# Kernel tuning notes

Measured on AMD Instinct MI355X. Metric: run time of the kernel, lower is better.

The kernel has to match this reference:

```python
import jax, jax.numpy as jnp
import numpy as np

N, T, D, H, E, ED = 4096, 16, 5, 128, 32768, 32

def _leaky(x):
    return jnp.where(x >= 0, x, 0.2 * x)

def _lstm(x, Wih, Whh, bih, bhh):
    # x: [N, T, D] -> hidden sequence [N, T, H]; PyTorch gate order i,f,g,o
    pre = jnp.einsum('ntd,gd->tng', x, Wih) + bih + bhh  # [T, N, 4H]
    Hd = Whh.shape[1]
    def step(carry, p):
        h, c = carry
        g = p + h @ Whh.T
        i, f, gg, o = jnp.split(g, 4, axis=-1)
        c = jax.nn.sigmoid(f) * c + jax.nn.sigmoid(i) * jnp.tanh(gg)
        h = jax.nn.sigmoid(o) * jnp.tanh(c)
        return (h, c), h
    z = jnp.zeros((x.shape[0], Hd), x.dtype)
    _, hs = jax.lax.scan(step, (z, z), pre)
    return jnp.swapaxes(hs, 0, 1)

def _sire(x, src, dst, efeat, Wq, bq, Wk, bk, We, be, Wr, br):
    # SIREConv with agg_type='sum': m = LeakyReLU(eq[dst]+ek[src]+e); sum over in-edges; then linear_relation
    eq = x @ Wq.T + bq            # [N, T, H]
    ek = x @ Wk.T + bk            # [N, T, H]
    e = efeat @ We.T + be         # [E, H]
    m = _leaky(eq[dst] + ek[src] + e[:, None, :])  # [E, T, H]
    ft = jax.ops.segment_sum(m, dst, num_segments=x.shape[0])  # [N, T, H]
    return ft @ Wr.T + br

def _forward(stock_features, srcs, dsts, efeats, sire_ps, lstm_p, attn_p, mlp_p):
    sf = stock_features / jnp.mean(stock_features, axis=1, keepdims=True)
    sr = _lstm(sf, *lstm_p)  # [N, T, H]
    outs = [sr]
    for s, d, ef, p in zip(srcs, dsts, efeats, sire_ps):
        outs.append(_sire(sr, s, d, ef, *p))
    cat = jnp.concatenate(outs, axis=-1)  # [N, T, 4H]
    aw = jax.nn.softmax(cat @ attn_p[0].T + attn_p[1], axis=-2)  # softmax over time
    pooled = jnp.sum(cat * aw, axis=-2)   # [N, 4H]
    W1, b1, W2, b2 = mlp_p
    h = _leaky(pooled @ W1.T + b1)
    out = _leaky(h @ W2.T + b2)           # [N, 1]
    return out / sf[:, -1, 0:1] - 1.0


def setup_inputs() -> dict:
    key = jax.random.key(0)
    ks = iter(jax.random.split(key, 64))
    def nrm(shape, s=0.05):
        return jax.random.normal(next(ks), shape, jnp.float32) * s
    inp = {}
    inp['stock_features'] = jax.random.uniform(next(ks), (N, T, D), jnp.float32) + 0.5
    for g in ['wiki', 'industry', 'corr']:
        inp[g + '_src'] = jax.random.randint(next(ks), (E,), 0, N, jnp.int32)
        inp[g + '_dst'] = jax.random.randint(next(ks), (E,), 0, N, jnp.int32)
        inp[g + '_efeat'] = nrm((E, ED), 1.0)
        inp[g + '_Wq'] = nrm((H, H)); inp[g + '_bq'] = nrm((H,))
        inp[g + '_Wk'] = nrm((H, H)); inp[g + '_bk'] = nrm((H,))
        inp[g + '_We'] = nrm((H, ED)); inp[g + '_be'] = nrm((H,))
        inp[g + '_Wr'] = nrm((H, H)); inp[g + '_br'] = nrm((H,))
    inp['lstm_Wih'] = nrm((4 * H, D)); inp['lstm_Whh'] = nrm((4 * H, H))
    inp['lstm_bih'] = nrm((4 * H,)); inp['lstm_bhh'] = nrm((4 * H,))
    inp['attn_W'] = nrm((1, 4 * H)); inp['attn_b'] = nrm((1,))
    inp['mlp_W1'] = nrm((H, 4 * H)); inp['mlp_b1'] = nrm((H,))
    inp['mlp_W2'] = nrm((1, H)); inp['mlp_b2'] = nrm((1,))
    return inp


def reference(stock_features, wiki_src, wiki_dst, wiki_efeat,
              wiki_Wq, wiki_bq, wiki_Wk, wiki_bk, wiki_We, wiki_be, wiki_Wr, wiki_br,
              industry_src, industry_dst, industry_efeat,
              industry_Wq, industry_bq, industry_Wk, industry_bk, industry_We, industry_be, industry_Wr, industry_br,
              corr_src, corr_dst, corr_efeat,
              corr_Wq, corr_bq, corr_Wk, corr_bk, corr_We, corr_be, corr_Wr, corr_br,
              lstm_Wih, lstm_Whh, lstm_bih, lstm_bhh,
              attn_W, attn_b, mlp_W1, mlp_b1, mlp_W2, mlp_b2):
    srcs = (wiki_src, industry_src, corr_src)
    dsts = (wiki_dst, industry_dst, corr_dst)
    efeats = (wiki_efeat, industry_efeat, corr_efeat)
    sire_ps = ((wiki_Wq, wiki_bq, wiki_Wk, wiki_bk, wiki_We, wiki_be, wiki_Wr, wiki_br),
               (industry_Wq, industry_bq, industry_Wk, industry_bk, industry_We, industry_be, industry_Wr, industry_br),
               (corr_Wq, corr_bq, corr_Wk, corr_bk, corr_We, corr_be, corr_Wr, corr_br))
    return _forward(stock_features, srcs, dsts, efeats, sire_ps,
                    (lstm_Wih, lstm_Whh, lstm_bih, lstm_bhh),
                    (attn_W, attn_b), (mlp_W1, mlp_b1, mlp_W2, mlp_b2))
```

## Files before the change

### kernel.cpp

```cpp
#include <hip/hip_runtime.h>
#include <cstdint>
#include <cstddef>

#define NS 4096
#define TS 16
#define DF 5
#define HD 128
#define EE 32768
#define EDD 32

typedef _Float16 h16;
typedef __attribute__((ext_vector_type(8))) _Float16 f16x8;
typedef __attribute__((ext_vector_type(2))) __fp16 fp16x2_n;
typedef __attribute__((ext_vector_type(4))) float f32x4;

__device__ __forceinline__ float sigmoidf_(float x){ return 1.f/(1.f+__expf(-x)); }
__device__ __forceinline__ float tanhf_(float x){ return 1.f - 2.f/(1.f+__expf(2.f*x)); }
__device__ __forceinline__ float leaky_(float x){ return x >= 0.f ? x : 0.2f*x; }

__device__ __forceinline__ unsigned pkh(float a, float b){
  union { fp16x2_n h; unsigned u; } x;
  x.h = __builtin_amdgcn_cvt_pkrtz(a, b);
  return x.u;
}
__device__ __forceinline__ void unpkh(unsigned u, float& a, float& b){
  union { unsigned u; fp16x2_n h; } x; x.u = u;
  a = (float)x.h.x; b = (float)x.h.y;
}
__device__ __forceinline__ f16x8 ld_h8(const h16* p){
  union { uint4 u; f16x8 v; } x; x.u = *(const uint4*)p; return x.v;
}

template<int AH, int CH>
__device__ __forceinline__ void gemm_dev(const void* Av, int lda,
    const float* __restrict__ Bp, int ldb, const float* __restrict__ bp,
    void* Cv, int ldc, int K, int act, size_t m0,
    h16* Asb, h16* Bsb)
{
  int tid = threadIdx.x;
  int wv = tid>>6, lane = tid&63, lm = lane&15, lq = lane>>4;
  f32x4 acc[2][8];
  #pragma unroll
  for (int mt=0;mt<2;mt++)
    #pragma unroll
    for (int nt=0;nt<8;nt++)
      acc[mt][nt] = (f32x4){0.f,0.f,0.f,0.f};

  for (int k0=0; k0<K; k0+=32){
    if (AH){
      const h16* A = (const h16*)Av;
      #pragma unroll
      for (int rep=0;rep<2;rep++){
        int idx = tid + rep*256;
        int row = idx>>2, c8 = idx&3;
        *(uint4*)&Asb[row*40 + c8*8] = *(const uint4*)&A[(m0+row)*(size_t)lda + k0 + c8*8];
      }
    } else {
      const float* A = (const float*)Av;
      #pragma unroll
      for (int rep=0;rep<4;rep++){
        int idx = tid + rep*256;
        int row = idx>>3, c4 = idx&7;
        float4 a = *(const float4*)&A[(m0+row)*(size_t)lda + k0 + c4*4];
        *(uint2*)&Asb[row*40 + c4*4] = make_uint2(pkh(a.x,a.y), pkh(a.z,a.w));
      }
    }
    #pragma unroll
    for (int rep=0;rep<4;rep++){
      int idx = tid + rep*256;
      int row = idx>>3, c4 = idx&7;
      float4 b = *(const float4*)&Bp[(size_t)row*ldb + k0 + c4*4];
      *(uint2*)&Bsb[row*40 + c4*4] = make_uint2(pkh(b.x,b.y), pkh(b.z,b.w));
    }
    __syncthreads();
    f16x8 afr[2], bfr[8];
    #pragma unroll
    for (int mt=0;mt<2;mt++)
      afr[mt] = ld_h8(&Asb[(wv*32 + mt*16 + lm)*40 + lq*8]);
    #pragma unroll
    for (int nt=0;nt<8;nt++)
      bfr[nt] = ld_h8(&Bsb[(nt*16 + lm)*40 + lq*8]);
    #pragma unroll
    for (int mt=0;mt<2;mt++)
      #pragma unroll
      for (int nt=0;nt<8;nt++)
        acc[mt][nt] = __builtin_amdgcn_mfma_f32_16x16x32_f16(afr[mt], bfr[nt], acc[mt][nt], 0,0,0);
    __syncthreads();
  }

  #pragma unroll
  for (int mt=0;mt<2;mt++){
    #pragma unroll
    for (int nt=0;nt<8;nt++){
      int col = nt*16 + lm;
      float bv = bp[col];
      #pragma unroll
      for (int i=0;i<4;i++){
        float o = acc[mt][nt][i] + bv;
        if (act) o = leaky_(o);
        size_t ridx = (m0 + wv*32 + mt*16 + lq*4 + i)*(size_t)ldc + col;
        if (CH) ((h16*)Cv)[ridx] = (h16)o;
        else    ((float*)Cv)[ridx] = o;
      }
    }
  }
}

__device__ void lstm8_dev(int blk, const float* __restrict__ sf,
                          const h16* __restrict__ WhhH,
                          const float* __restrict__ Wih, const float* __restrict__ bih,
                          const float* __restrict__ bhh, h16* __restrict__ srG,
                          char* smem)
{
  float* gates = (float*)smem;
  h16* hbuf = (h16*)(smem+16512);
  float* sfb = (float*)(smem+16512+2176);
  int tid = threadIdx.x;
  int n0 = blk*8;
  int wv = tid>>6, lane = tid&63, lm = lane&15, lq = lane>>4;

  f16x8 bfr[8][4];
  #pragma unroll
  for (int nt=0;nt<8;nt++){
    int g = wv*128 + nt*16 + lm;
    #pragma unroll
    for (int kt=0;kt<4;kt++)
      bfr[nt][kt] = *(const f16x8*)&WhhH[g*128 + kt*32 + lq*8];
  }

  int j = tid & 127;
  int rb = tid >> 7;
  float wih[4][5]; float bsum[4];
  #pragma unroll
  for (int gi=0; gi<4; gi++){
    int gc = gi*128 + j;
    #pragma unroll
    for (int d=0; d<5; d++) wih[gi][d] = Wih[gc*5+d];
    bsum[gi] = bih[gc] + bhh[gc];
  }
  float cst[4] = {0.f,0.f,0.f,0.f};

  for (int i=tid;i<544;i+=256) ((unsigned*)hbuf)[i] = 0;
  for (int i=tid;i<640;i+=256) sfb[i] = sf[(size_t)n0*80 + i];
  __syncthreads();

  f16x8 zf = {0,0,0,0,0,0,0,0};
  for (int t=0;t<16;t++){
    f16x8 af[4];
    #pragma unroll
    for (int kt=0;kt<4;kt++)
      af[kt] = (lm < 8) ? *(const f16x8*)&hbuf[lm*136 + kt*32 + lq*8] : zf;
    #pragma unroll
    for (int nt=0;nt<8;nt++){
      f32x4 acc = {0.f,0.f,0.f,0.f};
      #pragma unroll
      for (int kt=0;kt<4;kt++)
        acc = __builtin_amdgcn_mfma_f32_16x16x32_f16(af[kt], bfr[nt][kt], acc, 0,0,0);
      if (lq < 2){
        int col = wv*128 + nt*16 + lm;
        #pragma unroll
        for (int i=0;i<4;i++)
          gates[(lq*4+i)*516 + col] = acc[i];
      }
    }
    __syncthreads();
    #pragma unroll
    for (int q=0;q<4;q++){
      int r = rb + 2*q;
      const float* s = &sfb[r*80 + t*5];
      float pre[4];
      #pragma unroll
      for (int gi=0;gi<4;gi++){
        float a = bsum[gi];
        #pragma unroll
        for (int d=0;d<5;d++) a = fmaf(s[d], wih[gi][d], a);
        pre[gi] = a + gates[r*516 + gi*128 + j];
      }
      float iv = sigmoidf_(pre[0]);
      float fv = sigmoidf_(pre[1]);
      float gv = tanhf_(pre[2]);
      float ov = sigmoidf_(pre[3]);
      float c = fv*cst[q] + iv*gv;
      cst[q] = c;
      float h = ov*tanhf_(c);
      h16 hh = (h16)h;
      hbuf[r*136 + j] = hh;
      srG[(size_t)((n0+r)*16 + t)*128 + j] = hh;
    }
    __syncthreads();
  }
}

struct PP { const float* Wr[3]; };
__global__ __launch_bounds__(256)
void k_prolog(const float* __restrict__ x, float* __restrict__ sf,
              const float* __restrict__ Whh, h16* __restrict__ whhH,
              int* __restrict__ cnt, PP wr, h16* __restrict__ wrH)
{
  int b = blockIdx.x, tid = threadIdx.x;
  if (b < 48){
    int i = b*256 + tid;
    if (i < 3*4096) cnt[i] = 0;
  } else if (b < 128){
    int id = (b-48)*256 + tid;
    if (id < NS*DF){
      int n = id / DF, d = id % DF;
      const float* xp = x + (size_t)n*TS*DF + d;
      float s = 0.f;
      #pragma unroll
      for (int t=0;t<TS;t++) s += xp[t*DF];
      float inv = (float)TS / s;
      float* sp = sf + (size_t)n*TS*DF + d;
      #pragma unroll
      for (int t=0;t<TS;t++) sp[t*DF] = xp[t*DF]*inv;
    }
  } else if (b < 384){
    int i = (b-128)*256 + tid;
    whhH[i] = (h16)Whh[i];
  } else {
    int i = (b-384)*256 + tid;
    int g = i >> 14, r = i & 16383;
    wrH[i] = (h16)wr.Wr[g][r];
  }
}

struct M1 {
  const float *sf, *Wih, *bih, *bhh;
  const h16* WhhH;
  h16* srG;
  const float *ef[3]; const float *We[3]; const float *be[3];
  h16* eeb;
  const int* dst[3]; const int* src[3];
  int* cnt;
  int2* eidx2;
};
__global__ __launch_bounds__(256,2)
void k_mega1(M1 p)
{
  __shared__ __align__(16) char smem[21504];
  int b = blockIdx.x;
  if (b < 512){
    lstm8_dev(b, p.sf, p.WhhH, p.Wih, p.bih, p.bhh, p.srG, smem);
  } else if (b < 1280){
    int idx = b - 512;
    int proj = idx % 3, mt = idx / 3;
    h16* Asb = (h16*)smem;
    h16* Bsb = Asb + 128*40;
    gemm_dev<0,1>(p.ef[proj], 32, p.We[proj], 32, p.be[proj],
                  p.eeb + (size_t)proj*EE*128, 128, 32, 0, (size_t)mt*128, Asb, Bsb);
  } else {
    int idx = b - 1280;
    int g = idx >> 7, blk = idx & 127;
    int e = blk*256 + threadIdx.x;
    int d = p.dst[g][e];
    int s = p.src[g][e];
    int pos = atomicAdd(&p.cnt[g*4096 + d], 1);
    if (pos < 32) p.eidx2[((size_t)(g*4096 + d))*32 + pos] = make_int2(e, s);
  }
}

struct M2 {
  const h16* srG;
  const float* W[6]; const float* bias[6];
  h16* eqk;
};
__global__ __launch_bounds__(256)
void k_mega2(M2 p)
{
  __shared__ __align__(16) h16 Asb[128*40];
  __shared__ __align__(16) h16 Bsb[128*40];
  int b = blockIdx.x;
  int proj = b % 6, mt = b / 6;
  gemm_dev<1,1>(p.srG, 128, p.W[proj], 128, p.bias[proj],
                p.eqk + (size_t)proj*NS*TS*128, 128, 128, 0, (size_t)mt*128, Asb, Bsb);
}

struct EWP { const float* br[3]; };
__global__ __launch_bounds__(256)
void k_edgeattn(const h16* __restrict__ srG, const h16* __restrict__ eqk,
                const h16* __restrict__ eeb, const int* __restrict__ cnt,
                const int2* __restrict__ eidx2, const h16* __restrict__ wrH,
                EWP wp, const float* __restrict__ attnW,
                const float* __restrict__ attnB, h16* __restrict__ pooled)
{
  __shared__ __align__(16) h16 ctS[16*520];
  __shared__ __align__(16) h16 ftS[16*136];
  __shared__ float sred[4][16];
  int n = blockIdx.x;
  int tid = threadIdx.x;
  int wv = tid>>6, lane = tid&63, lm = lane&15, lq = lane>>4;
  int t = tid>>4, hb = (tid&15)*8;

  *(uint4*)&ctS[t*520 + hb] = *(const uint4*)&srG[((size_t)(n*16+t))*128 + hb];

  const f16x8 c02 = {(h16)0.2f,(h16)0.2f,(h16)0.2f,(h16)0.2f,
                     (h16)0.2f,(h16)0.2f,(h16)0.2f,(h16)0.2f};

  for (int g=0; g<3; g++){
    const h16* eqb = eqk + (size_t)(2*g)  *NS*TS*128;
    const h16* ekb = eqk + (size_t)(2*g+1)*NS*TS*128;
    const h16* eeg = eeb + (size_t)g*EE*128;

    size_t own = ((size_t)(n*16+t))*128 + hb;
    f16x8 eqv = ld_h8(&eqb[own]);
    float acc[8];
    #pragma unroll
    for (int j=0;j<8;j++) acc[j]=0.f;
    int ne = cnt[g*4096 + n]; if (ne > 32) ne = 32;
    const int2* el = eidx2 + ((size_t)(g*4096 + n))*32;
    for (int i=0;i<ne;i++){
      int2 es = el[i];
      f16x8 kv = ld_h8(&ekb[((size_t)(es.y*16+t))*128 + hb]);
      f16x8 ev = ld_h8(&eeg[(size_t)es.x*128 + hb]);
      f16x8 x = eqv + kv + ev;
      f16x8 lk = __builtin_elementwise_max(x, x*c02);
      #pragma unroll
      for (int j=0;j<8;j++) acc[j] += (float)lk[j];
    }
    uint4 o;
    o.x = pkh(acc[0],acc[1]); o.y = pkh(acc[2],acc[3]);
    o.z = pkh(acc[4],acc[5]); o.w = pkh(acc[6],acc[7]);
    *(uint4*)&ftS[t*136 + hb] = o;
    __syncthreads();

    f16x8 af[4];
    #pragma unroll
    for (int kt=0;kt<4;kt++)
      af[kt] = ld_h8(&ftS[lm*136 + kt*32 + lq*8]);
    const h16* wrg = wrH + (size_t)g*128*128;
    const float* br = wp.br[g];
    #pragma unroll
    for (int nn=0; nn<2; nn++){
      int nt = wv*2 + nn;
      f32x4 a2 = {0.f,0.f,0.f,0.f};
      #pragma unroll
      for (int kt=0;kt<4;kt++){
        f16x8 bf = ld_h8(&wrg[(nt*16+lm)*128 + kt*32 + lq*8]);
        a2 = __builtin_amdgcn_mfma_f32_16x16x32_f16(af[kt], bf, a2, 0,0,0);
      }
      int colg = (1+g)*128 + nt*16 + lm;
      float bv = br[nt*16 + lm];
      #pragma unroll
      for (int i=0;i<4;i++)
        ctS[(lq*4+i)*520 + colg] = (h16)(a2[i] + bv);
    }
    __syncthreads();
  }

  int c0 = tid*2;
  float w0 = attnW[c0], w1 = attnW[c0+1];
  const unsigned* ctu = (const unsigned*)ctS;
  float loc[16];
  #pragma unroll
  for (int tt=0;tt<16;tt++){
    float a,b; unpkh(ctu[tt*260 + tid], a, b);
    loc[tt] = a*w0 + b*w1;
  }
  #pragma unroll
  for (int tt=0;tt<16;tt++){
    float v = loc[tt];
    for (int off=1; off<64; off<<=1) v += __shfl_xor(v, off, 64);
    loc[tt]=v;
  }
  if (lane==0){
    #pragma unroll
    for (int tt=0;tt<16;tt++) sred[wv][tt]=loc[tt];
  }
  __syncthreads();
  float s[16]; float m=-1e30f;
  float ab = attnB[0];
  #pragma unroll
  for (int tt=0;tt<16;tt++){ s[tt] = sred[0][tt]+sred[1][tt]+sred[2][tt]+sred[3][tt] + ab; m = fmaxf(m, s[tt]); }
  float sum=0.f;
  #pragma unroll
  for (int tt=0;tt<16;tt++){ s[tt] = __expf(s[tt]-m); sum += s[tt]; }
  float inv = 1.f/sum;
  float p0=0.f,p1=0.f;
  #pragma unroll
  for (int tt=0;tt<16;tt++){
    float a = s[tt]*inv;
    float x,y; unpkh(ctu[tt*260 + tid], x, y);
    p0 = fmaf(x, a, p0); p1 = fmaf(y, a, p1);
  }
  ((unsigned*)pooled)[(size_t)n*256 + tid] = pkh(p0,p1);
}

__global__ __launch_bounds__(256)
void k_mlp(const h16* __restrict__ pooled, const float* __restrict__ W1,
           const float* __restrict__ b1, h16* __restrict__ hmlp,
           const float* __restrict__ W2, const float* __restrict__ b2,
           const float* __restrict__ sf, float* __restrict__ out)
{
  __shared__ __align__(16) h16 Asb[128*40];
  __shared__ __align__(16) h16 Bsb[128*40];
  size_t m0 = (size_t)blockIdx.x*128;
  gemm_dev<1,1>(pooled, 512, W1, 512, b1, hmlp, 128, 512, 1, m0, Asb, Bsb);
  __syncthreads();
  int tid = threadIdx.x;
  int r = tid >> 1, o64 = (tid & 1)*64;
  const h16* hp = hmlp + (m0 + r)*128 + o64;
  float acc = 0.f;
  #pragma unroll
  for (int c=0; c<64; c++) acc = fmaf((float)hp[c], W2[o64 + c], acc);
  acc += __shfl_xor(acc, 1, 64);
  if ((tid & 1) == 0){
    float o = leaky_(acc + b2[0]);
    size_t n = m0 + r;
    out[n] = o / sf[n*80 + 75] - 1.f;
  }
}

extern "C" void kernel_launch(void* const* d_in, const int* in_sizes, int n_in,
                              void* d_out, int out_size, void* d_ws, size_t ws_size,
                              hipStream_t stream)
{
  const float* x    = (const float*)d_in[0];
  const float* Wih  = (const float*)d_in[34];
  const float* Whh  = (const float*)d_in[35];
  const float* bih  = (const float*)d_in[36];
  const float* bhh  = (const float*)d_in[37];
  const float* attnW= (const float*)d_in[38];
  const float* attnB= (const float*)d_in[39];
  const float* W1   = (const float*)d_in[40];
  const float* b1   = (const float*)d_in[41];
  const float* W2   = (const float*)d_in[42];
  const float* b2   = (const float*)d_in[43];

  char* w = (char*)d_ws;
  size_t o = 0;
  h16* srG    = (h16*)(w+o); o += (size_t)NS*TS*128*2;
  h16* eqk    = (h16*)(w+o); o += (size_t)6*NS*TS*128*2;
  h16* eeb    = (h16*)(w+o); o += (size_t)3*EE*128*2;
  h16* pooled = (h16*)(w+o); o += (size_t)NS*512*2;
  float* sf   = (float*)(w+o); o += (size_t)NS*TS*DF*4;
  h16* hmlp   = (h16*)(w+o); o += (size_t)NS*HD*2;
  h16* whhH   = (h16*)(w+o); o += (size_t)512*128*2;
  h16* wrH    = (h16*)(w+o); o += (size_t)3*128*128*2;
  int* cnt    = (int*)(w+o); o += 3*4096*4;
  int2* eidx2 = (int2*)(w+o); o += (size_t)3*4096*32*8;

  {
    PP pp;
    for (int g=0; g<3; g++) pp.Wr[g] = (const float*)d_in[1 + g*11 + 9];
    k_prolog<<<576, 256, 0, stream>>>(x, sf, Whh, whhH, cnt, pp, wrH);
  }

  {
    M1 p;
    p.sf = sf; p.Wih = Wih; p.bih = bih; p.bhh = bhh;
    p.WhhH = whhH; p.srG = srG; p.eeb = eeb; p.cnt = cnt; p.eidx2 = eidx2;
    for (int g=0; g<3; g++){
      int base = 1 + g*11;
      p.src[g] = (const int*)d_in[base+0];
      p.dst[g] = (const int*)d_in[base+1];
      p.ef[g] = (const float*)d_in[base+2];
      p.We[g] = (const float*)d_in[base+7];
      p.be[g] = (const float*)d_in[base+8];
    }
    k_mega1<<<1664, 256, 0, stream>>>(p);
  }

  {
    M2 p;
    p.srG = srG; p.eqk = eqk;
    for (int g=0; g<3; g++){
      int base = 1 + g*11;
      p.W[2*g]      = (const float*)d_in[base+3];
      p.bias[2*g]   = (const float*)d_in[base+4];
      p.W[2*g+1]    = (const float*)d_in[base+5];
      p.bias[2*g+1] = (const float*)d_in[base+6];
    }
    k_mega2<<<3072, 256, 0, stream>>>(p);
  }

  {
    EWP wp;
    for (int g=0; g<3; g++) wp.br[g] = (const float*)d_in[1 + g*11 + 10];
    k_edgeattn<<<NS, 256, 0, stream>>>(srG, eqk, eeb, cnt, eidx2, wrH, wp,
                                       attnW, attnB, pooled);
  }

  k_mlp<<<32, 256, 0, stream>>>(pooled, W1, b1, hmlp, W2, b2, sf, (float*)d_out);
}
```

Baseline: 349.5 us.

## Assign one wavefront per graph in edge aggregation kernel

Restructures the per-node edge aggregation so each of three wavefronts handles one relation graph concurrently, with the fourth wave copying the LSTM hidden state. Each lane now covers 32 hidden channels instead of 8, and each wave runs all eight MFMA output tiles for its own graph's Wr projection. This drops the serial per-graph loop and its barriers, leaving two syncs instead of six. In exchange, per-lane register use grows (32 accumulators plus 4 eq vectors), wave 3 does little work, and gather loads per lane are less spread across lanes.

Result: slower. 382.4 us (+9.4%).

```diff
diff --git a/kernel.cpp b/kernel.cpp
--- a/kernel.cpp
+++ b/kernel.cpp
@@ -284,54 +284,72 @@
                 const float* __restrict__ attnB, h16* __restrict__ pooled)
 {
   __shared__ __align__(16) h16 ctS[16*520];
-  __shared__ __align__(16) h16 ftS[16*136];
+  __shared__ __align__(16) h16 ftS[3][16*136];
   __shared__ float sred[4][16];
   int n = blockIdx.x;
   int tid = threadIdx.x;
   int wv = tid>>6, lane = tid&63, lm = lane&15, lq = lane>>4;
-  int t = tid>>4, hb = (tid&15)*8;
-
-  *(uint4*)&ctS[t*520 + hb] = *(const uint4*)&srG[((size_t)(n*16+t))*128 + hb];
-
-  const f16x8 c02 = {(h16)0.2f,(h16)0.2f,(h16)0.2f,(h16)0.2f,
-                     (h16)0.2f,(h16)0.2f,(h16)0.2f,(h16)0.2f};
-
-  for (int g=0; g<3; g++){
+
+  if (wv == 3){
+    #pragma unroll
+    for (int j=0;j<4;j++){
+      int idx = j*64 + lane;
+      int t = idx>>4, ho = (idx&15)*8;
+      *(uint4*)&ctS[t*520 + ho] = *(const uint4*)&srG[((size_t)(n*16+t))*128 + ho];
+    }
+  } else {
+    int g = wv;
     const h16* eqb = eqk + (size_t)(2*g)  *NS*TS*128;
     const h16* ekb = eqk + (size_t)(2*g+1)*NS*TS*128;
     const h16* eeg = eeb + (size_t)g*EE*128;
-
-    size_t own = ((size_t)(n*16+t))*128 + hb;
-    f16x8 eqv = ld_h8(&eqb[own]);
-    float acc[8];
-    #pragma unroll
-    for (int j=0;j<8;j++) acc[j]=0.f;
+    int t = lane>>2, co = (lane&3)*32;
+    size_t ownr = ((size_t)(n*16+t))*128 + co;
+    f16x8 eqv[4];
+    #pragma unroll
+    for (int j=0;j<4;j++) eqv[j] = ld_h8(&eqb[ownr + j*8]);
+    const f16x8 c02 = {(h16)0.2f,(h16)0.2f,(h16)0.2f,(h16)0.2f,
+                       (h16)0.2f,(h16)0.2f,(h16)0.2f,(h16)0.2f};
+    float acc[4][8];
+    #pragma unroll
+    for (int j=0;j<4;j++)
+      #pragma unroll
+      for (int k=0;k<8;k++) acc[j][k]=0.f;
     int ne = cnt[g*4096 + n]; if (ne > 32) ne = 32;
     const int2* el = eidx2 + ((size_t)(g*4096 + n))*32;
     for (int i=0;i<ne;i++){
       int2 es = el[i];
-      f16x8 kv = ld_h8(&ekb[((size_t)(es.y*16+t))*128 + hb]);
-      f16x8 ev = ld_h8(&eeg[(size_t)es.x*128 + hb]);
-      f16x8 x = eqv + kv + ev;
-      f16x8 lk = __builtin_elementwise_max(x, x*c02);
-      #pragma unroll
-      for (int j=0;j<8;j++) acc[j] += (float)lk[j];
-    }
-    uint4 o;
-    o.x = pkh(acc[0],acc[1]); o.y = pkh(acc[2],acc[3]);
-    o.z = pkh(acc[4],acc[5]); o.w = pkh(acc[6],acc[7]);
-    *(uint4*)&ftS[t*136 + hb] = o;
-    __syncthreads();
-
+      const h16* kp = &ekb[((size_t)(es.y*16+t))*128 + co];
+      const h16* ep = &eeg[(size_t)es.x*128 + co];
+      #pragma unroll
+      for (int j=0;j<4;j++){
+        f16x8 kv = ld_h8(&kp[j*8]);
+        f16x8 ev = ld_h8(&ep[j*8]);
+        f16x8 x = eqv[j] + kv + ev;
+        f16x8 lk = __builtin_elementwise_max(x, x*c02);
+        #pragma unroll
+        for (int k=0;k<8;k++) acc[j][k] += (float)lk[k];
+      }
+    }
+    #pragma unroll
+    for (int j=0;j<4;j++){
+      uint4 o;
+      o.x = pkh(acc[j][0],acc[j][1]); o.y = pkh(acc[j][2],acc[j][3]);
+      o.z = pkh(acc[j][4],acc[j][5]); o.w = pkh(acc[j][6],acc[j][7]);
+      *(uint4*)&ftS[g][t*136 + co + j*8] = o;
+    }
+  }
+  __syncthreads();
+
+  if (wv < 3){
+    int g = wv;
     f16x8 af[4];
     #pragma unroll
     for (int kt=0;kt<4;kt++)
-      af[kt] = ld_h8(&ftS[lm*136 + kt*32 + lq*8]);
+      af[kt] = ld_h8(&ftS[g][lm*136 + kt*32 + lq*8]);
     const h16* wrg = wrH + (size_t)g*128*128;
     const float* br = wp.br[g];
     #pragma unroll
-    for (int nn=0; nn<2; nn++){
-      int nt = wv*2 + nn;
+    for (int nt=0; nt<8; nt++){
       f32x4 a2 = {0.f,0.f,0.f,0.f};
       #pragma unroll
       for (int kt=0;kt<4;kt++){
@@ -344,8 +362,8 @@
       for (int i=0;i<4;i++)
         ctS[(lq*4+i)*520 + colg] = (h16)(a2[i] + bv);
     }
-    __syncthreads();
-  }
+  }
+  __syncthreads();
 
   int c0 = tid*2;
   float w0 = attnW[c0], w1 = attnW[c0+1];
```

## Merge per-graph edge loops into one loop and drop per-graph barriers

Applied to the files above, without the earlier changes.

The three per-graph edge-aggregation loops become a single loop over all of a node's in-edges, with separate accumulators per graph, so the block hits one barrier instead of two per graph. Aggregated features now go straight into the concat shared buffer, which removes the separate staging array. Three waves then each run one graph's relation projection over all 8 output tiles, in place. The trade-off is that the graph index is chosen per edge at runtime, so the accumulators and query vectors are indexed dynamically. That can push them into scratch memory or add select chains, and one wave sits idle during the projection.

Result: slower. 890.5 us (+154.8%).

```diff
diff --git a/kernel.cpp b/kernel.cpp
--- a/kernel.cpp
+++ b/kernel.cpp
@@ -284,7 +284,6 @@
                 const float* __restrict__ attnB, h16* __restrict__ pooled)
 {
   __shared__ __align__(16) h16 ctS[16*520];
-  __shared__ __align__(16) h16 ftS[16*136];
   __shared__ float sred[4][16];
   int n = blockIdx.x;
   int tid = threadIdx.x;
@@ -293,45 +292,58 @@
 
   *(uint4*)&ctS[t*520 + hb] = *(const uint4*)&srG[((size_t)(n*16+t))*128 + hb];
 
+  size_t own = ((size_t)(n*16+t))*128 + hb;
+  f16x8 eqv[3];
+  #pragma unroll
+  for (int g=0; g<3; g++)
+    eqv[g] = ld_h8(&eqk[(size_t)(2*g)*NS*TS*128 + own]);
+
+  int ne0 = cnt[n];        if (ne0 > 32) ne0 = 32;
+  int ne1 = cnt[4096 + n]; if (ne1 > 32) ne1 = 32;
+  int ne2 = cnt[8192 + n]; if (ne2 > 32) ne2 = 32;
+  int neT = ne0 + ne1 + ne2;
+
   const f16x8 c02 = {(h16)0.2f,(h16)0.2f,(h16)0.2f,(h16)0.2f,
                      (h16)0.2f,(h16)0.2f,(h16)0.2f,(h16)0.2f};
-
-  for (int g=0; g<3; g++){
-    const h16* eqb = eqk + (size_t)(2*g)  *NS*TS*128;
-    const h16* ekb = eqk + (size_t)(2*g+1)*NS*TS*128;
-    const h16* eeg = eeb + (size_t)g*EE*128;
-
-    size_t own = ((size_t)(n*16+t))*128 + hb;
-    f16x8 eqv = ld_h8(&eqb[own]);
-    float acc[8];
-    #pragma unroll
-    for (int j=0;j<8;j++) acc[j]=0.f;
-    int ne = cnt[g*4096 + n]; if (ne > 32) ne = 32;
-    const int2* el = eidx2 + ((size_t)(g*4096 + n))*32;
-    for (int i=0;i<ne;i++){
-      int2 es = el[i];
-      f16x8 kv = ld_h8(&ekb[((size_t)(es.y*16+t))*128 + hb]);
-      f16x8 ev = ld_h8(&eeg[(size_t)es.x*128 + hb]);
-      f16x8 x = eqv + kv + ev;
-      f16x8 lk = __builtin_elementwise_max(x, x*c02);
-      #pragma unroll
-      for (int j=0;j<8;j++) acc[j] += (float)lk[j];
-    }
+  float acc[3][8];
+  #pragma unroll
+  for (int g=0;g<3;g++)
+    #pragma unroll
+    for (int k=0;k<8;k++) acc[g][k]=0.f;
+
+  for (int i=0;i<neT;i++){
+    int g, idx;
+    if (i < ne0)            { g=0; idx=i; }
+    else if (i < ne0 + ne1) { g=1; idx=i-ne0; }
+    else                    { g=2; idx=i-ne0-ne1; }
+    int2 es = eidx2[((size_t)(g*4096 + n))*32 + idx];
+    f16x8 kv = ld_h8(&eqk[(size_t)(2*g+1)*NS*TS*128 + ((size_t)(es.y*16+t))*128 + hb]);
+    f16x8 ev = ld_h8(&eeb[(size_t)g*EE*128 + (size_t)es.x*128 + hb]);
+    f16x8 x = eqv[g] + kv + ev;
+    f16x8 lk = __builtin_elementwise_max(x, x*c02);
+    #pragma unroll
+    for (int k=0;k<8;k++) acc[g][k] += (float)lk[k];
+  }
+
+  #pragma unroll
+  for (int g=0;g<3;g++){
     uint4 o;
-    o.x = pkh(acc[0],acc[1]); o.y = pkh(acc[2],acc[3]);
-    o.z = pkh(acc[4],acc[5]); o.w = pkh(acc[6],acc[7]);
-    *(uint4*)&ftS[t*136 + hb] = o;
-    __syncthreads();
-
+    o.x = pkh(acc[g][0],acc[g][1]); o.y = pkh(acc[g][2],acc[g][3]);
+    o.z = pkh(acc[g][4],acc[g][5]); o.w = pkh(acc[g][6],acc[g][7]);
+    *(uint4*)&ctS[t*520 + (1+g)*128 + hb] = o;
+  }
+  __syncthreads();
+
+  if (wv < 3){
+    int g = wv;
     f16x8 af[4];
     #pragma unroll
     for (int kt=0;kt<4;kt++)
-      af[kt] = ld_h8(&ftS[lm*136 + kt*32 + lq*8]);
+      af[kt] = ld_h8(&ctS[lm*520 + (1+g)*128 + kt*32 + lq*8]);
     const h16* wrg = wrH + (size_t)g*128*128;
     const float* br = wp.br[g];
     #pragma unroll
-    for (int nn=0; nn<2; nn++){
-      int nt = wv*2 + nn;
+    for (int nt=0; nt<8; nt++){
       f32x4 a2 = {0.f,0.f,0.f,0.f};
       #pragma unroll
       for (int kt=0;kt<4;kt++){
@@ -344,8 +356,8 @@
       for (int i=0;i<4;i++)
         ctS[(lq*4+i)*520 + colg] = (h16)(a2[i] + bv);
     }
-    __syncthreads();
-  }
+  }
+  __syncthreads();
 
   int c0 = tid*2;
   float w0 = attnW[c0], w1 = attnW[c0+1];
```

## Batch the three graph gathers before one barrier and split relation GEMMs across waves

Applied to the files above, without the earlier changes.

The edge-attention kernel now runs the gather-and-aggregate loops for all three graphs back to back, writing each aggregate straight into its column slice of the shared concat buffer. The separate ftS buffer goes away, and the per-graph pair of barriers becomes one barrier before and one after the relation projection. In that projection, waves 0–2 each handle all eight output tiles for one graph while wave 3 sits idle. The aim is fewer block-wide syncs, more independent gather loads in flight per thread, and less LDS use, at the cost of an uneven split of the MFMA phase and higher register pressure.

New measurement: 374.4 us. 1.07x slower.

```diff
diff --git a/kernel.cpp b/kernel.cpp
--- a/kernel.cpp
+++ b/kernel.cpp
@@ -284,7 +284,6 @@
                 const float* __restrict__ attnB, h16* __restrict__ pooled)
 {
   __shared__ __align__(16) h16 ctS[16*520];
-  __shared__ __align__(16) h16 ftS[16*136];
   __shared__ float sred[4][16];
   int n = blockIdx.x;
   int tid = threadIdx.x;
@@ -293,45 +292,52 @@
 
   *(uint4*)&ctS[t*520 + hb] = *(const uint4*)&srG[((size_t)(n*16+t))*128 + hb];
 
+  size_t own = ((size_t)(n*16+t))*128 + hb;
   const f16x8 c02 = {(h16)0.2f,(h16)0.2f,(h16)0.2f,(h16)0.2f,
                      (h16)0.2f,(h16)0.2f,(h16)0.2f,(h16)0.2f};
 
-  for (int g=0; g<3; g++){
-    const h16* eqb = eqk + (size_t)(2*g)  *NS*TS*128;
-    const h16* ekb = eqk + (size_t)(2*g+1)*NS*TS*128;
-    const h16* eeg = eeb + (size_t)g*EE*128;
-
-    size_t own = ((size_t)(n*16+t))*128 + hb;
-    f16x8 eqv = ld_h8(&eqb[own]);
-    float acc[8];
-    #pragma unroll
-    for (int j=0;j<8;j++) acc[j]=0.f;
-    int ne = cnt[g*4096 + n]; if (ne > 32) ne = 32;
-    const int2* el = eidx2 + ((size_t)(g*4096 + n))*32;
-    for (int i=0;i<ne;i++){
-      int2 es = el[i];
-      f16x8 kv = ld_h8(&ekb[((size_t)(es.y*16+t))*128 + hb]);
-      f16x8 ev = ld_h8(&eeg[(size_t)es.x*128 + hb]);
-      f16x8 x = eqv + kv + ev;
-      f16x8 lk = __builtin_elementwise_max(x, x*c02);
-      #pragma unroll
-      for (int j=0;j<8;j++) acc[j] += (float)lk[j];
-    }
-    uint4 o;
-    o.x = pkh(acc[0],acc[1]); o.y = pkh(acc[2],acc[3]);
-    o.z = pkh(acc[4],acc[5]); o.w = pkh(acc[6],acc[7]);
-    *(uint4*)&ftS[t*136 + hb] = o;
-    __syncthreads();
-
+  #define GATHER(G, ACC)                                                        \
+  {                                                                             \
+    const h16* eqb = eqk + (size_t)(2*(G))*NS*TS*128;                           \
+    const h16* ekb = eqk + (size_t)(2*(G)+1)*NS*TS*128;                         \
+    const h16* eeg = eeb + (size_t)(G)*EE*128;                                  \
+    f16x8 eqv = ld_h8(&eqb[own]);                                               \
+    int ne = cnt[(G)*4096 + n]; if (ne > 32) ne = 32;                           \
+    const int2* el = eidx2 + ((size_t)((G)*4096 + n))*32;                       \
+    for (int i=0;i<ne;i++){                                                     \
+      int2 es = el[i];                                                          \
+      f16x8 kv = ld_h8(&ekb[((size_t)(es.y*16+t))*128 + hb]);                   \
+      f16x8 ev = ld_h8(&eeg[(size_t)es.x*128 + hb]);                            \
+      f16x8 x = eqv + kv + ev;                                                  \
+      f16x8 lk = __builtin_elementwise_max(x, x*c02);                           \
+      _Pragma("unroll")                                                         \
+      for (int k=0;k<8;k++) ACC[k] += (float)lk[k];                             \
+    }                                                                           \
+    uint4 o;                                                                    \
+    o.x = pkh(ACC[0],ACC[1]); o.y = pkh(ACC[2],ACC[3]);                         \
+    o.z = pkh(ACC[4],ACC[5]); o.w = pkh(ACC[6],ACC[7]);                         \
+    *(uint4*)&ctS[t*520 + (1+(G))*128 + hb] = o;                                \
+  }
+
+  float acc0[8], acc1[8], acc2[8];
+  #pragma unroll
+  for (int k=0;k<8;k++){ acc0[k]=0.f; acc1[k]=0.f; acc2[k]=0.f; }
+  GATHER(0, acc0)
+  GATHER(1, acc1)
+  GATHER(2, acc2)
+  #undef GATHER
+  __syncthreads();
+
+  if (wv < 3){
+    int g = wv;
     f16x8 af[4];
     #pragma unroll
     for (int kt=0;kt<4;kt++)
-      af[kt] = ld_h8(&ftS[lm*136 + kt*32 + lq*8]);
+      af[kt] = ld_h8(&ctS[lm*520 + (1+g)*128 + kt*32 + lq*8]);
     const h16* wrg = wrH + (size_t)g*128*128;
     const float* br = wp.br[g];
     #pragma unroll
-    for (int nn=0; nn<2; nn++){
-      int nt = wv*2 + nn;
+    for (int nt=0; nt<8; nt++){
       f32x4 a2 = {0.f,0.f,0.f,0.f};
       #pragma unroll
       for (int kt=0;kt<4;kt++){
@@ -344,8 +350,8 @@
       for (int i=0;i<4;i++)
         ctS[(lq*4+i)*520 + colg] = (h16)(a2[i] + bv);
     }
-    __syncthreads();
-  }
+  }
+  __syncthreads();
 
   int c0 = tid*2;
   float w0 = attnW[c0], w1 = attnW[c0+1];
```
